# Performance work log

Measured on AMD Instinct MI355X. Metric: run time of the kernel, lower is better.

## Reference

```python
import jax, jax.numpy as jnp
import numpy as np

ALPHAS = [2.0 ** k for k in range(-3, 2)]  # default GaussianKernel bandwidth magnitudes


def _cdist(x, y):
    # Euclidean distance matrix with torch.cdist-compatible zero-distance subgradient.
    sq = (jnp.sum(x * x, axis=1)[:, None]
          + jnp.sum(y * y, axis=1)[None, :]
          - 2.0 * (x @ y.T))
    sq = jnp.maximum(sq, 0.0)
    safe = jnp.where(sq > 0, sq, 1.0)
    return jnp.where(sq > 0, jnp.sqrt(safe), 0.0)


def setup_inputs() -> dict:
    key = jax.random.key(0)
    k1, k2 = jax.random.split(key)
    xs = jax.random.normal(k1, (4096, 256), dtype=jnp.float32)
    xt = jax.random.normal(k2, (4096, 256), dtype=jnp.float32)
    return {"xs": xs, "xt": xt}


def reference(xs, xt):
    xs = xs.reshape(xs.shape[0], -1)
    xt = xt.reshape(xt.shape[0], -1)
    b = xs.shape[0]

    # Compute the three pairwise distance matrices ONCE (the torch loop redoes
    # this per kernel; the math is identical).
    dxx = _cdist(xs, xs)  # [B, B]
    dyy = _cdist(xt, xt)
    dxy = _cdist(xs, xt)

    # sigma^2 = alpha * mean(dist), with the mean detached (stop_gradient).
    mxx = jax.lax.stop_gradient(jnp.mean(dxx))
    myy = jax.lax.stop_gradient(jnp.mean(dyy))
    mxy = jax.lax.stop_gradient(jnp.mean(dxy))

    total = jnp.zeros_like(dxx)
    for a in ALPHAS:
        kxx = jnp.exp(-dxx / (2.0 * a * mxx))
        kyy = jnp.exp(-dyy / (2.0 * a * myy))
        kxy = jnp.exp(-dxy / (2.0 * a * mxy))
        total = total + (kxx + kyy - 2.0 * kxy)

    loss = jnp.sqrt(jnp.sum(total) / (b * (b - 1.0)))
    return jnp.where(jnp.isnan(loss), jnp.zeros_like(loss), loss)
```

## Files before the change

### kernel.cpp

```cpp
#include <hip/hip_runtime.h>

#define BN 4096
#define KD 256
#define TILE 128
#define BK 64

typedef short bf16x8 __attribute__((ext_vector_type(8)));
typedef float f32x4 __attribute__((ext_vector_type(4)));
typedef _Float16 h2 __attribute__((ext_vector_type(2)));
typedef unsigned short ushort_t;
typedef unsigned int uint_t;

#define NSLOT 2080

__device__ inline void async_load16(const void* g, void* l) {
    __builtin_amdgcn_global_load_lds((const __attribute__((address_space(1))) void*)g,
                                     (__attribute__((address_space(3))) void*)l,
                                     16, 0, 0);
}

__device__ inline ushort_t f2bf(float f) {
    union { float f; unsigned int u; } x;
    x.f = f;
    unsigned int u = x.u;
    unsigned int r = (u + 0x7fffu + ((u >> 16) & 1u)) >> 16;
    return (ushort_t)r;
}

__device__ __forceinline__ float fast_sqrt(float x) {
    return __builtin_amdgcn_sqrtf(x);
}
__device__ __forceinline__ float fast_exp2(float x) {
    return __builtin_amdgcn_exp2f(x);
}

__device__ __forceinline__ void decode_slot(int slot, int& z, int& bi, int& bj) {
    if (slot >= 1056) {
        z = 2; int t = slot - 1056; bi = t >> 5; bj = t & 31;
    } else {
        z = (slot >= 528) ? 1 : 0;
        int t = slot - z * 528;
        int b = (int)(32.5f - sqrtf(1056.25f - 2.0f * (float)t));
        while (b * (65 - b) / 2 > t) --b;
        while ((b + 1) * (64 - b) / 2 <= t) ++b;
        bi = b;
        bj = bi + (t - bi * (65 - bi) / 2);
    }
}

__global__ __launch_bounds__(256) void norm_cvt(
        const float* __restrict__ xs, const float* __restrict__ xt,
        ushort_t* __restrict__ xsb, ushort_t* __restrict__ xtb,
        float* __restrict__ norms) {
    int w = threadIdx.x >> 6;
    int lane = threadIdx.x & 63;
    int row = blockIdx.x * 4 + w;
    const float* src = (row < BN) ? xs + (size_t)row * KD
                                  : xt + (size_t)(row - BN) * KD;
    ushort_t* dst = (row < BN) ? xsb + (size_t)row * KD
                               : xtb + (size_t)(row - BN) * KD;
    float4 v = ((const float4*)src)[lane];
    float s = v.x * v.x + v.y * v.y + v.z * v.z + v.w * v.w;
#pragma unroll
    for (int off = 32; off > 0; off >>= 1) s += __shfl_xor(s, off, 64);
    if (lane == 0) norms[row] = s;
    ushort4 o;
    o.x = f2bf(v.x); o.y = f2bf(v.y); o.z = f2bf(v.z); o.w = f2bf(v.w);
    ((ushort4*)dst)[lane] = o;
}


template <bool DIAG>
__device__ __forceinline__ float epilogue_store(
        const f32x4 (&acc)[4][4], const float* nxv, const float* nyv,
        int wr, int wc, int q, int m16, int tid, uint_t* __restrict__ tileBase) {
    float local = 0.0f;
    uint4* tb4 = (uint4*)tileBase;
#pragma unroll
    for (int rg = 0; rg < 4; ++rg) {
#pragma unroll
        for (int np = 0; np < 2; ++np) {
            uint_t packed[4];
#pragma unroll
            for (int ngh = 0; ngh < 2; ++ngh) {
                int ng = np * 2 + ngh;
#pragma unroll
                for (int rp = 0; rp < 2; ++rp) {
                    float dpair[2];
#pragma unroll
                    for (int rh = 0; rh < 2; ++rh) {
                        int rr = rp * 2 + rh;
                        float sq = nxv[rg * 4 + rr] + nyv[ng] - 2.0f * acc[rg][ng][rr];
                        sq = fmaxf(sq, 0.0f);
                        float d = fast_sqrt(sq);
                        if (DIAG) {
                            int i = wr * 64 + rg * 16 + q * 4 + rr;
                            int j = wc * 64 + ng * 16 + m16;
                            if (i == j) d = 0.0f;
                        }
                        local += d;
                        dpair[rh] = d;
                    }
                    h2 p;
                    p[0] = (_Float16)dpair[0];
                    p[1] = (_Float16)dpair[1];
                    packed[ngh * 2 + rp] = __builtin_bit_cast(uint_t, p);
                }
            }
            uint4 v;
            v.x = packed[0]; v.y = packed[1]; v.z = packed[2]; v.w = packed[3];
            tb4[(rg * 2 + np) * 256 + tid] = v;
        }
    }
    return local;
}

__global__ __launch_bounds__(256) void mmd_pass1(
        const ushort_t* __restrict__ xsb, const ushort_t* __restrict__ xtb,
        const float* __restrict__ norms, float* __restrict__ partialArr,
        uint_t* __restrict__ dbuf) {
    const int slot = blockIdx.x;
    int z, bi, bj;
    decode_slot(slot, z, bi, bj);

    const ushort_t* X = (z == 1) ? xtb : xsb;
    const ushort_t* Y = (z == 0) ? xsb : xtb;
    const float* nX = norms + ((z == 1) ? BN : 0);
    const float* nY = norms + ((z == 0) ? 0 : BN);

    const int tid = threadIdx.x;
    const int lane = tid & 63;
    const int w = tid >> 6;
    const int wr = w >> 1;
    const int wc = w & 1;
    const int m16 = lane & 15;
    const int q = lane >> 4;

    const int i0 = bi * TILE;
    const int j0 = bj * TILE;

    __shared__ ushort_t lA[TILE * BK];
    __shared__ ushort_t lB[TILE * BK];
    __shared__ float red[4];

    f32x4 acc[4][4] = {};

#pragma unroll
    for (int kk = 0; kk < KD; kk += BK) {
        __syncthreads();
#pragma unroll
        for (int t = 0; t < 4; ++t) {
            int rowblk = w * 4 + t;
            int r = rowblk * 8 + (lane >> 3);
            int cch = lane & 7;
            int gch = cch ^ (r & 7);
            const ushort_t* gA = X + (size_t)(i0 + r) * KD + (kk + gch * 8);
            const ushort_t* gB = Y + (size_t)(j0 + r) * KD + (kk + gch * 8);
            async_load16(gA, (char*)lA + rowblk * 1024);
            async_load16(gB, (char*)lB + rowblk * 1024);
        }
        __syncthreads();

#pragma unroll
        for (int ks = 0; ks < 2; ++ks) {
            bf16x8 af[4], bfr[4];
            int kap = ks * 4 + q;
#pragma unroll
            for (int rg = 0; rg < 4; ++rg) {
                int rowa = wr * 64 + rg * 16 + m16;
                int posa = kap ^ (rowa & 7);
                af[rg] = *(const bf16x8*)&lA[rowa * BK + posa * 8];
                int rowb = wc * 64 + rg * 16 + m16;
                int posb = kap ^ (rowb & 7);
                bfr[rg] = *(const bf16x8*)&lB[rowb * BK + posb * 8];
            }
#pragma unroll
            for (int rg = 0; rg < 4; ++rg)
#pragma unroll
                for (int ng = 0; ng < 4; ++ng)
                    acc[rg][ng] = __builtin_amdgcn_mfma_f32_16x16x32_bf16(
                        af[rg], bfr[ng], acc[rg][ng], 0, 0, 0);
        }
    }

    float nxv[16];
#pragma unroll
    for (int rg = 0; rg < 4; ++rg)
#pragma unroll
        for (int rr = 0; rr < 4; ++rr)
            nxv[rg * 4 + rr] = nX[i0 + wr * 64 + rg * 16 + q * 4 + rr];
    float nyv[4];
#pragma unroll
    for (int ng = 0; ng < 4; ++ng)
        nyv[ng] = nY[j0 + wc * 64 + ng * 16 + m16];

    uint_t* tileBase = dbuf + (size_t)slot * 8192;
    float local;
    if (z < 2 && bi == bj)
        local = epilogue_store<true>(acc, nxv, nyv, wr, wc, q, m16, tid, tileBase);
    else
        local = epilogue_store<false>(acc, nxv, nyv, wr, wc, q, m16, tid, tileBase);

#pragma unroll
    for (int off = 32; off > 0; off >>= 1) local += __shfl_xor(local, off, 64);
    if (lane == 0) red[w] = local;
    __syncthreads();
    if (tid == 0) {
        float bs = red[0] + red[1] + red[2] + red[3];
        float c1 = (z < 2 && bi != bj) ? 2.0f : 1.0f;
        partialArr[slot] = c1 * bs;
    }
}


__global__ __launch_bounds__(256) void mmd_reduce1(
        const float* __restrict__ partialArr, double* __restrict__ sums) {
    const int tid = threadIdx.x;
    double a0 = 0.0, a1 = 0.0, a2 = 0.0;
    for (int s = tid; s < NSLOT; s += 256) {
        double v = (double)partialArr[s];
        if (s < 528) a0 += v; else if (s < 1056) a1 += v; else a2 += v;
    }
    const int lane = tid & 63, w = tid >> 6;
#pragma unroll
    for (int off = 32; off > 0; off >>= 1) {
        a0 += __shfl_xor(a0, off, 64);
        a1 += __shfl_xor(a1, off, 64);
        a2 += __shfl_xor(a2, off, 64);
    }
    __shared__ double r[4][3];
    if (lane == 0) { r[w][0] = a0; r[w][1] = a1; r[w][2] = a2; }
    __syncthreads();
    if (tid == 0) {
        sums[0] = r[0][0] + r[1][0] + r[2][0] + r[3][0];
        sums[1] = r[0][1] + r[1][1] + r[2][1] + r[3][1];
        sums[2] = r[0][2] + r[1][2] + r[2][2] + r[3][2];
    }
}


__global__ __launch_bounds__(256) void mmd_pass2(
        const uint_t* __restrict__ dbuf, const double* __restrict__ sums,
        float* __restrict__ partialArr) {
    const int tid = threadIdx.x;
    const int slot = blockIdx.x;
    const int lane = tid & 63;
    const int w = tid >> 6;
    int z, bi, bj;
    decode_slot(slot, z, bi, bj);
    double mz = sums[z] * (1.0 / 16777216.0);
    float nhb = (float)(-1.4426950408889634 / (4.0 * mz));
    float coef = (z == 2) ? -2.0f : ((bi != bj) ? 2.0f : 1.0f);
    const uint_t* base = dbuf + (size_t)slot * 8192;

    float local = 0.0f;
#pragma unroll
    for (int it = 0; it < 8; ++it) {
        uint4 v = ((const uint4*)base)[it * 256 + tid];
        uint_t arr[4] = {v.x, v.y, v.z, v.w};
#pragma unroll
        for (int j = 0; j < 4; ++j) {
            h2 p = __builtin_bit_cast(h2, arr[j]);
#pragma unroll
            for (int h = 0; h < 2; ++h) {
                float d = (float)p[h];
                float u = fast_exp2(d * nhb);
                float u2 = u * u;
                float u4 = u2 * u2;
                float u8 = u4 * u4;
                float u16 = u8 * u8;
                local += (u + u2) + (u4 + u8) + u16;
            }
        }
    }

    __shared__ float red[4];
#pragma unroll
    for (int off = 32; off > 0; off >>= 1) local += __shfl_xor(local, off, 64);
    if (lane == 0) red[w] = local;
    __syncthreads();
    if (tid == 0) {
        float bs = red[0] + red[1] + red[2] + red[3];
        partialArr[slot] = coef * bs;
    }
}


__global__ __launch_bounds__(256) void mmd_finalize2(
        const float* __restrict__ partialArr, float* __restrict__ out) {
    const int tid = threadIdx.x;
    double acc = 0.0;
    for (int s = tid; s < NSLOT; s += 256) acc += (double)partialArr[s];
    const int lane = tid & 63, w = tid >> 6;
#pragma unroll
    for (int off = 32; off > 0; off >>= 1) acc += __shfl_xor(acc, off, 64);
    __shared__ double r[4];
    if (lane == 0) r[w] = acc;
    __syncthreads();
    if (tid == 0) {
        double S = r[0] + r[1] + r[2] + r[3];
        double l = sqrt(S / ((double)BN * (double)(BN - 1)));
        float f = (float)l;
        if (!(f == f)) f = 0.0f;
        out[0] = f;
    }
}


template <int PASS>
__global__ __launch_bounds__(256) void mmd_gemm(
        const ushort_t* __restrict__ xsb, const ushort_t* __restrict__ xtb,
        const float* __restrict__ norms, double* __restrict__ sums) {
    const int z = blockIdx.z;
    const int bi = blockIdx.y;
    const int bj = blockIdx.x;
    if (z < 2 && bj < bi) return;

    const ushort_t* X = (z == 1) ? xtb : xsb;
    const ushort_t* Y = (z == 0) ? xsb : xtb;
    const float* nX = norms + ((z == 1) ? BN : 0);
    const float* nY = norms + ((z == 0) ? 0 : BN);

    const int tid = threadIdx.x;
    const int lane = tid & 63;
    const int w = tid >> 6;
    const int wr = w >> 1;
    const int wc = w & 1;
    const int m16 = lane & 15;
    const int q = lane >> 4;

    const int i0 = bi * TILE;
    const int j0 = bj * TILE;

    __shared__ ushort_t lA[TILE * BK];
    __shared__ ushort_t lB[TILE * BK];
    __shared__ float red[4];

    float nhb = 0.0f;
    if (PASS == 2) {
        double mz = sums[z] / ((double)BN * (double)BN);
        nhb = (float)(-1.4426950408889634 / (4.0 * mz));
    }

    f32x4 acc[4][4] = {};

#pragma unroll
    for (int kk = 0; kk < KD; kk += BK) {
        __syncthreads();
#pragma unroll
        for (int t = 0; t < 4; ++t) {
            int rowblk = w * 4 + t;
            int r = rowblk * 8 + (lane >> 3);
            int cch = lane & 7;
            int gch = cch ^ (r & 7);
            const ushort_t* gA = X + (size_t)(i0 + r) * KD + (kk + gch * 8);
            const ushort_t* gB = Y + (size_t)(j0 + r) * KD + (kk + gch * 8);
            async_load16(gA, (char*)lA + rowblk * 1024);
            async_load16(gB, (char*)lB + rowblk * 1024);
        }
        __syncthreads();

#pragma unroll
        for (int ks = 0; ks < 2; ++ks) {
            bf16x8 af[4], bfr[4];
            int kap = ks * 4 + q;
#pragma unroll
            for (int rg = 0; rg < 4; ++rg) {
                int rowa = wr * 64 + rg * 16 + m16;
                int posa = kap ^ (rowa & 7);
                af[rg] = *(const bf16x8*)&lA[rowa * BK + posa * 8];
                int rowb = wc * 64 + rg * 16 + m16;
                int posb = kap ^ (rowb & 7);
                bfr[rg] = *(const bf16x8*)&lB[rowb * BK + posb * 8];
            }
#pragma unroll
            for (int rg = 0; rg < 4; ++rg)
#pragma unroll
                for (int ng = 0; ng < 4; ++ng)
                    acc[rg][ng] = __builtin_amdgcn_mfma_f32_16x16x32_bf16(
                        af[rg], bfr[ng], acc[rg][ng], 0, 0, 0);
        }
    }

    float nxv[16];
#pragma unroll
    for (int rg = 0; rg < 4; ++rg)
#pragma unroll
        for (int rr = 0; rr < 4; ++rr)
            nxv[rg * 4 + rr] = nX[i0 + wr * 64 + rg * 16 + q * 4 + rr];
    float nyv[4];
#pragma unroll
    for (int ng = 0; ng < 4; ++ng)
        nyv[ng] = nY[j0 + wc * 64 + ng * 16 + m16];

    float local = 0.0f;
#pragma unroll
    for (int rg = 0; rg < 4; ++rg) {
#pragma unroll
        for (int ng = 0; ng < 4; ++ng) {
#pragma unroll
            for (int rr = 0; rr < 4; ++rr) {
                int i = i0 + wr * 64 + rg * 16 + q * 4 + rr;
                int j = j0 + wc * 64 + ng * 16 + m16;
                float sq = nxv[rg * 4 + rr] + nyv[ng] - 2.0f * acc[rg][ng][rr];
                sq = fmaxf(sq, 0.0f);
                float d = fast_sqrt(sq);
                if (z < 2 && i == j) d = 0.0f;
                if (PASS == 1) {
                    local += d;
                } else {
                    float u = fast_exp2(d * nhb);
                    float u2 = u * u;
                    float u4 = u2 * u2;
                    float u8 = u4 * u4;
                    float u16 = u8 * u8;
                    local += u + u2 + u4 + u8 + u16;
                }
            }
        }
    }

#pragma unroll
    for (int off = 32; off > 0; off >>= 1) local += __shfl_xor(local, off, 64);
    if (lane == 0) red[w] = local;
    __syncthreads();
    if (tid == 0) {
        double bs = (double)red[0] + (double)red[1] + (double)red[2] + (double)red[3];
        double coef = (z < 2 && bi != bj) ? 2.0 : 1.0;
        if (PASS == 2 && z == 2) coef = -2.0;
        atomicAdd(&sums[PASS == 1 ? z : 3], coef * bs);
    }
}

__global__ void mmd_finalize(const double* __restrict__ sums, float* __restrict__ out) {
    double S = sums[3];
    double l = sqrt(S / ((double)BN * (double)(BN - 1)));
    float f = (float)l;
    if (!(f == f)) f = 0.0f;
    out[0] = f;
}

extern "C" void kernel_launch(void* const* d_in, const int* in_sizes, int n_in,
                              void* d_out, int out_size, void* d_ws, size_t ws_size,
                              hipStream_t stream) {
    const float* xs = (const float*)d_in[0];
    const float* xt = (const float*)d_in[1];
    float* out = (float*)d_out;

    char* ws = (char*)d_ws;
    double* sums = (double*)ws;
    float* norms = (float*)(ws + 64);
    float* partialArr = (float*)(ws + 32832);
    ushort_t* xsb = (ushort_t*)(ws + 41216);
    ushort_t* xtb = xsb + (size_t)BN * KD;
    uint_t* dbuf = (uint_t*)(ws + 4235520);

    size_t need_small = 4235520;
    size_t need_big = 4235520 + (size_t)NSLOT * 32768;

    if (ws_size < need_small) {
        (void)hipMemsetAsync(d_out, 0xC0, 4, stream);
        return;
    }

    norm_cvt<<<2048, 256, 0, stream>>>(xs, xt, xsb, xtb, norms);

    if (ws_size >= need_big) {
        mmd_pass1<<<NSLOT, 256, 0, stream>>>(xsb, xtb, norms, partialArr, dbuf);
        mmd_reduce1<<<1, 256, 0, stream>>>(partialArr, sums);
        mmd_pass2<<<NSLOT, 256, 0, stream>>>(dbuf, sums, partialArr);
        mmd_finalize2<<<1, 256, 0, stream>>>(partialArr, out);
    } else {
        (void)hipMemsetAsync(d_ws, 0, 64, stream);
        dim3 g(32, 32, 3);
        mmd_gemm<1><<<g, 256, 0, stream>>>(xsb, xtb, norms, sums);
        mmd_gemm<2><<<g, 256, 0, stream>>>(xsb, xtb, norms, sums);
        mmd_finalize<<<1, 1, 0, stream>>>(sums, out);
    }
}
```

Baseline: 116.1 us.

## Load GEMM fragments directly from global memory and fold reduce into pass2

The pass-1 GEMM drops its LDS staging and barriers, and each lane reads its bf16x8 MFMA fragments straight from global memory, relying on the cache for reuse. The separate single-block reduce kernel is removed: every pass-2 block re-reduces the 2080 partial sums itself to get its bandwidth, which saves one launch and a serial step. The risk is that uncoalesced, strided global loads in the GEMM and the reduction repeated in every pass-2 block cost more than the barriers and launch they replace.

```diff
diff --git a/kernel.cpp b/kernel.cpp
--- a/kernel.cpp
+++ b/kernel.cpp
@@ -117,7 +117,7 @@
 
 __global__ __launch_bounds__(256) void mmd_pass1(
         const ushort_t* __restrict__ xsb, const ushort_t* __restrict__ xtb,
-        const float* __restrict__ norms, float* __restrict__ partialArr,
+        const float* __restrict__ norms, float* __restrict__ partialA,
         uint_t* __restrict__ dbuf) {
     const int slot = blockIdx.x;
     int z, bi, bj;
@@ -139,40 +139,21 @@
     const int i0 = bi * TILE;
     const int j0 = bj * TILE;
 
-    __shared__ ushort_t lA[TILE * BK];
-    __shared__ ushort_t lB[TILE * BK];
-    __shared__ float red[4];
+    const ushort_t* aBase = X + (size_t)(i0 + wr * 64 + m16) * KD + q * 8;
+    const ushort_t* bBase = Y + (size_t)(j0 + wc * 64 + m16) * KD + q * 8;
 
     f32x4 acc[4][4] = {};
 
 #pragma unroll
-    for (int kk = 0; kk < KD; kk += BK) {
-        __syncthreads();
-#pragma unroll
-        for (int t = 0; t < 4; ++t) {
-            int rowblk = w * 4 + t;
-            int r = rowblk * 8 + (lane >> 3);
-            int cch = lane & 7;
-            int gch = cch ^ (r & 7);
-            const ushort_t* gA = X + (size_t)(i0 + r) * KD + (kk + gch * 8);
-            const ushort_t* gB = Y + (size_t)(j0 + r) * KD + (kk + gch * 8);
-            async_load16(gA, (char*)lA + rowblk * 1024);
-            async_load16(gB, (char*)lB + rowblk * 1024);
-        }
-        __syncthreads();
-
+    for (int kk = 0; kk < 4; ++kk) {
 #pragma unroll
         for (int ks = 0; ks < 2; ++ks) {
+            const int coff = kk * 64 + ks * 32;
             bf16x8 af[4], bfr[4];
-            int kap = ks * 4 + q;
 #pragma unroll
             for (int rg = 0; rg < 4; ++rg) {
-                int rowa = wr * 64 + rg * 16 + m16;
-                int posa = kap ^ (rowa & 7);
-                af[rg] = *(const bf16x8*)&lA[rowa * BK + posa * 8];
-                int rowb = wc * 64 + rg * 16 + m16;
-                int posb = kap ^ (rowb & 7);
-                bfr[rg] = *(const bf16x8*)&lB[rowb * BK + posb * 8];
+                af[rg]  = *(const bf16x8*)(aBase + (size_t)rg * 16 * KD + coff);
+                bfr[rg] = *(const bf16x8*)(bBase + (size_t)rg * 16 * KD + coff);
             }
 #pragma unroll
             for (int rg = 0; rg < 4; ++rg)
@@ -201,6 +182,7 @@
     else
         local = epilogue_store<false>(acc, nxv, nyv, wr, wc, q, m16, tid, tileBase);
 
+    __shared__ float red[4];
 #pragma unroll
     for (int off = 32; off > 0; off >>= 1) local += __shfl_xor(local, off, 64);
     if (lane == 0) red[w] = local;
@@ -208,47 +190,40 @@
     if (tid == 0) {
         float bs = red[0] + red[1] + red[2] + red[3];
         float c1 = (z < 2 && bi != bj) ? 2.0f : 1.0f;
-        partialArr[slot] = c1 * bs;
-    }
-}
-
-
-__global__ __launch_bounds__(256) void mmd_reduce1(
-        const float* __restrict__ partialArr, double* __restrict__ sums) {
-    const int tid = threadIdx.x;
-    double a0 = 0.0, a1 = 0.0, a2 = 0.0;
-    for (int s = tid; s < NSLOT; s += 256) {
-        double v = (double)partialArr[s];
-        if (s < 528) a0 += v; else if (s < 1056) a1 += v; else a2 += v;
-    }
-    const int lane = tid & 63, w = tid >> 6;
-#pragma unroll
-    for (int off = 32; off > 0; off >>= 1) {
-        a0 += __shfl_xor(a0, off, 64);
-        a1 += __shfl_xor(a1, off, 64);
-        a2 += __shfl_xor(a2, off, 64);
-    }
-    __shared__ double r[4][3];
-    if (lane == 0) { r[w][0] = a0; r[w][1] = a1; r[w][2] = a2; }
-    __syncthreads();
-    if (tid == 0) {
-        sums[0] = r[0][0] + r[1][0] + r[2][0] + r[3][0];
-        sums[1] = r[0][1] + r[1][1] + r[2][1] + r[3][1];
-        sums[2] = r[0][2] + r[1][2] + r[2][2] + r[3][2];
+        partialA[slot] = c1 * bs;
     }
 }
 
 
 __global__ __launch_bounds__(256) void mmd_pass2(
-        const uint_t* __restrict__ dbuf, const double* __restrict__ sums,
-        float* __restrict__ partialArr) {
+        const uint_t* __restrict__ dbuf, const float* __restrict__ partialA,
+        float* __restrict__ partialB) {
     const int tid = threadIdx.x;
     const int slot = blockIdx.x;
     const int lane = tid & 63;
     const int w = tid >> 6;
     int z, bi, bj;
     decode_slot(slot, z, bi, bj);
-    double mz = sums[z] * (1.0 / 16777216.0);
+
+    double a0 = 0.0, a1 = 0.0, a2 = 0.0;
+    for (int s = tid; s < NSLOT; s += 256) {
+        double v = (double)partialA[s];
+        if (s < 528) a0 += v; else if (s < 1056) a1 += v; else a2 += v;
+    }
+#pragma unroll
+    for (int off = 32; off > 0; off >>= 1) {
+        a0 += __shfl_xor(a0, off, 64);
+        a1 += __shfl_xor(a1, off, 64);
+        a2 += __shfl_xor(a2, off, 64);
+    }
+    __shared__ double rs[4][3];
+    if (lane == 0) { rs[w][0] = a0; rs[w][1] = a1; rs[w][2] = a2; }
+    __syncthreads();
+    double sz = (z == 0) ? rs[0][0] + rs[1][0] + rs[2][0] + rs[3][0]
+              : (z == 1) ? rs[0][1] + rs[1][1] + rs[2][1] + rs[3][1]
+                         : rs[0][2] + rs[1][2] + rs[2][2] + rs[3][2];
+
+    double mz = sz * (1.0 / 16777216.0);
     float nhb = (float)(-1.4426950408889634 / (4.0 * mz));
     float coef = (z == 2) ? -2.0f : ((bi != bj) ? 2.0f : 1.0f);
     const uint_t* base = dbuf + (size_t)slot * 8192;
@@ -281,16 +256,16 @@
     __syncthreads();
     if (tid == 0) {
         float bs = red[0] + red[1] + red[2] + red[3];
-        partialArr[slot] = coef * bs;
+        partialB[slot] = coef * bs;
     }
 }
 
 
 __global__ __launch_bounds__(256) void mmd_finalize2(
-        const float* __restrict__ partialArr, float* __restrict__ out) {
+        const float* __restrict__ partialB, float* __restrict__ out) {
     const int tid = threadIdx.x;
     double acc = 0.0;
-    for (int s = tid; s < NSLOT; s += 256) acc += (double)partialArr[s];
+    for (int s = tid; s < NSLOT; s += 256) acc += (double)partialB[s];
     const int lane = tid & 63, w = tid >> 6;
 #pragma unroll
     for (int off = 32; off > 0; off >>= 1) acc += __shfl_xor(acc, off, 64);
@@ -450,13 +425,14 @@
     char* ws = (char*)d_ws;
     double* sums = (double*)ws;
     float* norms = (float*)(ws + 64);
-    float* partialArr = (float*)(ws + 32832);
-    ushort_t* xsb = (ushort_t*)(ws + 41216);
+    float* partialA = (float*)(ws + 32832);
+    float* partialB = (float*)(ws + 41152);
+    ushort_t* xsb = (ushort_t*)(ws + 49536);
     ushort_t* xtb = xsb + (size_t)BN * KD;
-    uint_t* dbuf = (uint_t*)(ws + 4235520);
-
-    size_t need_small = 4235520;
-    size_t need_big = 4235520 + (size_t)NSLOT * 32768;
+    uint_t* dbuf = (uint_t*)(ws + 4243840);
+
+    size_t need_small = 4243840;
+    size_t need_big = 4243840 + (size_t)NSLOT * 32768;
 
     if (ws_size < need_small) {
         (void)hipMemsetAsync(d_out, 0xC0, 4, stream);
@@ -466,10 +442,9 @@
     norm_cvt<<<2048, 256, 0, stream>>>(xs, xt, xsb, xtb, norms);
 
     if (ws_size >= need_big) {
-        mmd_pass1<<<NSLOT, 256, 0, stream>>>(xsb, xtb, norms, partialArr, dbuf);
-        mmd_reduce1<<<1, 256, 0, stream>>>(partialArr, sums);
-        mmd_pass2<<<NSLOT, 256, 0, stream>>>(dbuf, sums, partialArr);
-        mmd_finalize2<<<1, 256, 0, stream>>>(partialArr, out);
+        mmd_pass1<<<NSLOT, 256, 0, stream>>>(xsb, xtb, norms, partialA, dbuf);
+        mmd_pass2<<<NSLOT, 256, 0, stream>>>(dbuf, partialA, partialB);
+        mmd_finalize2<<<1, 256, 0, stream>>>(partialB, out);
     } else {
         (void)hipMemsetAsync(d_ws, 0, 64, stream);
         dim3 g(32, 32, 3);
```

Result: slower. 159.8 us (+37.6%).
